# Kernel optimization log

Hardware: AMD Instinct MI355X
Metric: run time of the kernel (lower is better)

## Reference

```python
import jax, jax.numpy as jnp
import numpy as np

N_NODES = 100000
N_EDGES = 3200000
D_NODE = 128
D_EDGE = 16


def setup_inputs() -> dict:
    key = jax.random.key(0)
    k1, k2, k3, k4, k5, k6, k7 = jax.random.split(key, 7)
    nodes = jax.random.normal(k1, (N_NODES, D_NODE), dtype=jnp.float32)
    edges = jax.random.normal(k2, (N_EDGES, D_EDGE), dtype=jnp.float32)
    senders = jax.random.randint(k3, (N_EDGES,), 0, N_NODES, dtype=jnp.int32)
    receivers = jax.random.randint(k4, (N_EDGES,), 0, N_NODES, dtype=jnp.int32)
    w_node = jax.random.normal(k5, (), dtype=jnp.float32)
    w_edge = jax.random.normal(k6, (), dtype=jnp.float32)
    b_node = jax.random.normal(k7, (), dtype=jnp.float32)
    return {
        "nodes": nodes,
        "edges": edges,
        "senders": senders,
        "receivers": receivers,
        "w_node": w_node,
        "w_edge": w_edge,
        "b_node": b_node,
    }


def reference(nodes, edges, senders, receivers, w_node, w_edge, b_node):
    # gather sender node scalar feature (column 0): [E]
    sender_vals = nodes[senders, 0]
    edge_vals = edges[:, 0]  # [E]
    # per-edge message: scalar mult-add
    messages = w_edge * edge_vals + w_node * sender_vals  # [E]
    # scatter-add into receivers: [N]
    agg = jax.ops.segment_sum(messages, receivers, num_segments=nodes.shape[0])
    return w_node * nodes[:, 0] + agg + b_node
```

## Files before the change

kernel.cpp:

```cpp
#include <hip/hip_runtime.h>

#define N_NODES 100000
#define N_EDGES 3200000
#define D_NODE 128
#define D_EDGE 16

__global__ void tmp_init_out(const float* __restrict__ nodes,
                             const float* __restrict__ w_node,
                             const float* __restrict__ b_node,
                             float* __restrict__ out) {
    int i = blockIdx.x * blockDim.x + threadIdx.x;
    if (i < N_NODES) {
        out[i] = w_node[0] * nodes[(size_t)i * D_NODE] + b_node[0];
    }
}

__global__ void tmp_edge_scatter(const float* __restrict__ nodes,
                                 const float* __restrict__ edges,
                                 const int*   __restrict__ senders,
                                 const int*   __restrict__ receivers,
                                 const float* __restrict__ w_node,
                                 const float* __restrict__ w_edge,
                                 float* __restrict__ out) {
    const float wn = w_node[0];
    const float we = w_edge[0];
    int base = (blockIdx.x * blockDim.x + threadIdx.x) * 4;
    if (base + 3 < N_EDGES) {
        int4 s = *(const int4*)(senders + base);
        int4 r = *(const int4*)(receivers + base);
        float e0 = edges[(size_t)(base + 0) * D_EDGE];
        float e1 = edges[(size_t)(base + 1) * D_EDGE];
        float e2 = edges[(size_t)(base + 2) * D_EDGE];
        float e3 = edges[(size_t)(base + 3) * D_EDGE];
        float m0 = we * e0 + wn * nodes[(size_t)s.x * D_NODE];
        float m1 = we * e1 + wn * nodes[(size_t)s.y * D_NODE];
        float m2 = we * e2 + wn * nodes[(size_t)s.z * D_NODE];
        float m3 = we * e3 + wn * nodes[(size_t)s.w * D_NODE];
        atomicAdd(&out[r.x], m0);
        atomicAdd(&out[r.y], m1);
        atomicAdd(&out[r.z], m2);
        atomicAdd(&out[r.w], m3);
    } else {
        for (int e = base; e < N_EDGES; ++e) {
            float m = we * edges[(size_t)e * D_EDGE]
                    + wn * nodes[(size_t)senders[e] * D_NODE];
            atomicAdd(&out[receivers[e]], m);
        }
    }
}

extern "C" void kernel_launch(void* const* d_in, const int* in_sizes, int n_in,
                              void* d_out, int out_size, void* d_ws, size_t ws_size,
                              hipStream_t stream) {
    const float* nodes     = (const float*)d_in[0];
    const float* edges     = (const float*)d_in[1];
    const int*   senders   = (const int*)d_in[2];
    const int*   receivers = (const int*)d_in[3];
    const float* w_node    = (const float*)d_in[4];
    const float* w_edge    = (const float*)d_in[5];
    const float* b_node    = (const float*)d_in[6];
    float* out = (float*)d_out;

    {
        int threads = 256;
        int blocks = (N_NODES + threads - 1) / threads;
        tmp_init_out<<<blocks, threads, 0, stream>>>(nodes, w_node, b_node, out);
    }
    {
        int threads = 256;
        int n_thr = N_EDGES / 4;
        int blocks = (n_thr + threads - 1) / threads;
        tmp_edge_scatter<<<blocks, threads, 0, stream>>>(
            nodes, edges, senders, receivers, w_node, w_edge, out);
    }
}
```

Before: 425.8 us.

## Privatize scatter-add into replicated workspace copies, then reduce

Splits the atomic scatter across up to 16 zero-initialised copies of the output held in workspace, chosen per wavefront, and adds a final kernel that sums the copies with the node term. The aim is to reduce atomic contention on shared receiver addresses. In exchange it adds a zeroing pass and a reduction pass that reads every copy, plus extra memory traffic. It falls back to the original direct path when the workspace is too small.

```diff
diff --git a/kernel.cpp b/kernel.cpp
--- a/kernel.cpp
+++ b/kernel.cpp
@@ -5,26 +5,24 @@
 #define D_NODE 128
 #define D_EDGE 16
 
-__global__ void tmp_init_out(const float* __restrict__ nodes,
-                             const float* __restrict__ w_node,
-                             const float* __restrict__ b_node,
-                             float* __restrict__ out) {
+__global__ void tmp_zero_ws(float4* __restrict__ ws, int n4) {
     int i = blockIdx.x * blockDim.x + threadIdx.x;
-    if (i < N_NODES) {
-        out[i] = w_node[0] * nodes[(size_t)i * D_NODE] + b_node[0];
-    }
+    if (i < n4) ws[i] = make_float4(0.f, 0.f, 0.f, 0.f);
 }
 
-__global__ void tmp_edge_scatter(const float* __restrict__ nodes,
-                                 const float* __restrict__ edges,
-                                 const int*   __restrict__ senders,
-                                 const int*   __restrict__ receivers,
-                                 const float* __restrict__ w_node,
-                                 const float* __restrict__ w_edge,
-                                 float* __restrict__ out) {
+__global__ void tmp_edge_scatter_rep(const float* __restrict__ nodes,
+                                     const float* __restrict__ edges,
+                                     const int*   __restrict__ senders,
+                                     const int*   __restrict__ receivers,
+                                     const float* __restrict__ w_node,
+                                     const float* __restrict__ w_edge,
+                                     float* __restrict__ ws, int rmask) {
     const float wn = w_node[0];
     const float we = w_edge[0];
-    int base = (blockIdx.x * blockDim.x + threadIdx.x) * 4;
+    int t = blockIdx.x * blockDim.x + threadIdx.x;
+    int base = t * 4;
+    if (base >= N_EDGES) return;
+    float* dst = ws + (size_t)((t >> 6) & rmask) * N_NODES;
     if (base + 3 < N_EDGES) {
         int4 s = *(const int4*)(senders + base);
         int4 r = *(const int4*)(receivers + base);
@@ -36,14 +34,63 @@
         float m1 = we * e1 + wn * nodes[(size_t)s.y * D_NODE];
         float m2 = we * e2 + wn * nodes[(size_t)s.z * D_NODE];
         float m3 = we * e3 + wn * nodes[(size_t)s.w * D_NODE];
+        atomicAdd(&dst[r.x], m0);
+        atomicAdd(&dst[r.y], m1);
+        atomicAdd(&dst[r.z], m2);
+        atomicAdd(&dst[r.w], m3);
+    } else {
+        for (int e = base; e < N_EDGES; ++e) {
+            float m = we * edges[(size_t)e * D_EDGE]
+                    + wn * nodes[(size_t)senders[e] * D_NODE];
+            atomicAdd(&dst[receivers[e]], m);
+        }
+    }
+}
+
+__global__ void tmp_reduce_out(const float* __restrict__ nodes,
+                               const float* __restrict__ ws,
+                               const float* __restrict__ w_node,
+                               const float* __restrict__ b_node,
+                               float* __restrict__ out, int nrep) {
+    int i = blockIdx.x * blockDim.x + threadIdx.x;
+    if (i >= N_NODES) return;
+    float s = w_node[0] * nodes[(size_t)i * D_NODE] + b_node[0];
+    for (int r = 0; r < nrep; ++r) s += ws[(size_t)r * N_NODES + i];
+    out[i] = s;
+}
+
+__global__ void tmp_init_out(const float* __restrict__ nodes,
+                             const float* __restrict__ w_node,
+                             const float* __restrict__ b_node,
+                             float* __restrict__ out) {
+    int i = blockIdx.x * blockDim.x + threadIdx.x;
+    if (i < N_NODES) out[i] = w_node[0] * nodes[(size_t)i * D_NODE] + b_node[0];
+}
+
+__global__ void tmp_edge_scatter_direct(const float* __restrict__ nodes,
+                                        const float* __restrict__ edges,
+                                        const int*   __restrict__ senders,
+                                        const int*   __restrict__ receivers,
+                                        const float* __restrict__ w_node,
+                                        const float* __restrict__ w_edge,
+                                        float* __restrict__ out) {
+    const float wn = w_node[0];
+    const float we = w_edge[0];
+    int base = (blockIdx.x * blockDim.x + threadIdx.x) * 4;
+    if (base + 3 < N_EDGES) {
+        int4 s = *(const int4*)(senders + base);
+        int4 r = *(const int4*)(receivers + base);
+        float m0 = we * edges[(size_t)(base + 0) * D_EDGE] + wn * nodes[(size_t)s.x * D_NODE];
+        float m1 = we * edges[(size_t)(base + 1) * D_EDGE] + wn * nodes[(size_t)s.y * D_NODE];
+        float m2 = we * edges[(size_t)(base + 2) * D_EDGE] + wn * nodes[(size_t)s.z * D_NODE];
+        float m3 = we * edges[(size_t)(base + 3) * D_EDGE] + wn * nodes[(size_t)s.w * D_NODE];
         atomicAdd(&out[r.x], m0);
         atomicAdd(&out[r.y], m1);
         atomicAdd(&out[r.z], m2);
         atomicAdd(&out[r.w], m3);
     } else {
         for (int e = base; e < N_EDGES; ++e) {
-            float m = we * edges[(size_t)e * D_EDGE]
-                    + wn * nodes[(size_t)senders[e] * D_NODE];
+            float m = we * edges[(size_t)e * D_EDGE] + wn * nodes[(size_t)senders[e] * D_NODE];
             atomicAdd(&out[receivers[e]], m);
         }
     }
@@ -60,17 +107,41 @@
     const float* w_edge    = (const float*)d_in[5];
     const float* b_node    = (const float*)d_in[6];
     float* out = (float*)d_out;
+    float* ws  = (float*)d_ws;
 
+    int R = 0;
     {
+        size_t per = (size_t)N_NODES * sizeof(float);
+        if (ws_size >= per) {
+            R = 1;
+            while (R < 16 && (size_t)(R * 2) * per <= ws_size) R *= 2;
+        }
+    }
+
+    if (R > 0) {
+        {
+            int n4 = (R * N_NODES) / 4;
+            int threads = 256;
+            tmp_zero_ws<<<(n4 + threads - 1) / threads, threads, 0, stream>>>(
+                (float4*)ws, n4);
+        }
+        {
+            int threads = 256;
+            int n_thr = N_EDGES / 4;
+            tmp_edge_scatter_rep<<<(n_thr + threads - 1) / threads, threads, 0, stream>>>(
+                nodes, edges, senders, receivers, w_node, w_edge, ws, R - 1);
+        }
+        {
+            int threads = 256;
+            tmp_reduce_out<<<(N_NODES + threads - 1) / threads, threads, 0, stream>>>(
+                nodes, ws, w_node, b_node, out, R);
+        }
+    } else {
         int threads = 256;
-        int blocks = (N_NODES + threads - 1) / threads;
-        tmp_init_out<<<blocks, threads, 0, stream>>>(nodes, w_node, b_node, out);
-    }
-    {
-        int threads = 256;
+        tmp_init_out<<<(N_NODES + threads - 1) / threads, threads, 0, stream>>>(
+            nodes, w_node, b_node, out);
         int n_thr = N_EDGES / 4;
-        int blocks = (n_thr + threads - 1) / threads;
-        tmp_edge_scatter<<<blocks, threads, 0, stream>>>(
+        tmp_edge_scatter_direct<<<(n_thr + threads - 1) / threads, threads, 0, stream>>>(
             nodes, edges, senders, receivers, w_node, w_edge, out);
     }
 }
```

After: 427.4 us. Within noise of the previous version (+0.4%).

## Replace global atomic scatter with range-partitioned LDS accumulation and partial reduction

Applied to the files above, without the earlier changes.

Splits the work into four kernels. The first extracts column 0 of the nodes into a compact array. The second computes per-edge messages into a workspace buffer. The third has each block accumulate messages for one 16K-node receiver range in shared memory, using LDS atomics, and write a partial sum. The last sums the partials per node and adds the node term and bias. This removes the random global atomics to the output, at the cost of re-reading receivers and messages once per range and of extra workspace traffic. The new path runs only if the workspace is large enough; otherwise it falls back to the direct atomic kernel.

```diff
diff --git a/kernel.cpp b/kernel.cpp
--- a/kernel.cpp
+++ b/kernel.cpp
@@ -5,46 +5,113 @@
 #define D_NODE 128
 #define D_EDGE 16
 
+#define RANGE_BITS 14
+#define RANGE_SIZE (1 << RANGE_BITS)
+#define RANGE_MASK (RANGE_SIZE - 1)
+#define N_RANGES 7
+
+#define WS_X_OFF    0
+#define WS_MSG_OFF  102400
+#define WS_PART_OFF (102400 + N_EDGES)
+
+__global__ void tmp_k0_extract(const float* __restrict__ nodes,
+                               float* __restrict__ x) {
+    int i = blockIdx.x * blockDim.x + threadIdx.x;
+    if (i < N_NODES) x[i] = nodes[(size_t)i * D_NODE];
+}
+
+__global__ void tmp_k1_messages(const float* __restrict__ x,
+                                const float* __restrict__ edges,
+                                const int*   __restrict__ senders,
+                                const float* __restrict__ w_node,
+                                const float* __restrict__ w_edge,
+                                float* __restrict__ msg) {
+    const float wn = w_node[0];
+    const float we = w_edge[0];
+    int base = (blockIdx.x * blockDim.x + threadIdx.x) * 4;
+    if (base >= N_EDGES) return;
+    int4 s = *(const int4*)(senders + base);
+    float4 m;
+    m.x = we * edges[(size_t)(base + 0) * D_EDGE] + wn * x[s.x];
+    m.y = we * edges[(size_t)(base + 1) * D_EDGE] + wn * x[s.y];
+    m.z = we * edges[(size_t)(base + 2) * D_EDGE] + wn * x[s.z];
+    m.w = we * edges[(size_t)(base + 3) * D_EDGE] + wn * x[s.w];
+    *(float4*)(msg + base) = m;
+}
+
+__global__ void tmp_k2_accum(const float* __restrict__ msg,
+                             const int*   __restrict__ receivers,
+                             float* __restrict__ partials, int nb) {
+    extern __shared__ float acc[];
+    const int range = blockIdx.y;
+    const int slice = blockIdx.x;
+
+    for (int i = threadIdx.x; i < RANGE_SIZE; i += blockDim.x) acc[i] = 0.f;
+    __syncthreads();
+
+    int chunk = (N_EDGES + nb - 1) / nb;
+    chunk = (chunk + 3) & ~3;
+    int start = slice * chunk;
+    int end = start + chunk; if (end > N_EDGES) end = N_EDGES;
+
+    for (int e = start + (int)threadIdx.x * 4; e < end; e += (int)blockDim.x * 4) {
+        int4 r = *(const int4*)(receivers + e);
+        float4 m = *(const float4*)(msg + e);
+        if ((r.x >> RANGE_BITS) == range) atomicAdd(&acc[r.x & RANGE_MASK], m.x);
+        if ((r.y >> RANGE_BITS) == range) atomicAdd(&acc[r.y & RANGE_MASK], m.y);
+        if ((r.z >> RANGE_BITS) == range) atomicAdd(&acc[r.z & RANGE_MASK], m.z);
+        if ((r.w >> RANGE_BITS) == range) atomicAdd(&acc[r.w & RANGE_MASK], m.w);
+    }
+    __syncthreads();
+
+    float* dst = partials + ((size_t)(range * nb + slice) << RANGE_BITS);
+    for (int i = threadIdx.x; i < RANGE_SIZE; i += blockDim.x) dst[i] = acc[i];
+}
+
+__global__ void tmp_k3_reduce(const float* __restrict__ x,
+                              const float* __restrict__ partials,
+                              const float* __restrict__ w_node,
+                              const float* __restrict__ b_node,
+                              float* __restrict__ out, int nb) {
+    int i = blockIdx.x * blockDim.x + threadIdx.x;
+    if (i >= N_NODES) return;
+    int range = i >> RANGE_BITS;
+    int local = i & RANGE_MASK;
+    float s = w_node[0] * x[i] + b_node[0];
+    const float* p = partials + ((size_t)(range * nb) << RANGE_BITS) + local;
+    for (int b = 0; b < nb; ++b) s += p[(size_t)b << RANGE_BITS];
+    out[i] = s;
+}
+
 __global__ void tmp_init_out(const float* __restrict__ nodes,
                              const float* __restrict__ w_node,
                              const float* __restrict__ b_node,
                              float* __restrict__ out) {
     int i = blockIdx.x * blockDim.x + threadIdx.x;
-    if (i < N_NODES) {
-        out[i] = w_node[0] * nodes[(size_t)i * D_NODE] + b_node[0];
-    }
+    if (i < N_NODES) out[i] = w_node[0] * nodes[(size_t)i * D_NODE] + b_node[0];
 }
 
-__global__ void tmp_edge_scatter(const float* __restrict__ nodes,
-                                 const float* __restrict__ edges,
-                                 const int*   __restrict__ senders,
-                                 const int*   __restrict__ receivers,
-                                 const float* __restrict__ w_node,
-                                 const float* __restrict__ w_edge,
-                                 float* __restrict__ out) {
+__global__ void tmp_edge_scatter_direct(const float* __restrict__ nodes,
+                                        const float* __restrict__ edges,
+                                        const int*   __restrict__ senders,
+                                        const int*   __restrict__ receivers,
+                                        const float* __restrict__ w_node,
+                                        const float* __restrict__ w_edge,
+                                        float* __restrict__ out) {
     const float wn = w_node[0];
     const float we = w_edge[0];
     int base = (blockIdx.x * blockDim.x + threadIdx.x) * 4;
     if (base + 3 < N_EDGES) {
         int4 s = *(const int4*)(senders + base);
         int4 r = *(const int4*)(receivers + base);
-        float e0 = edges[(size_t)(base + 0) * D_EDGE];
-        float e1 = edges[(size_t)(base + 1) * D_EDGE];
-        float e2 = edges[(size_t)(base + 2) * D_EDGE];
-        float e3 = edges[(size_t)(base + 3) * D_EDGE];
-        float m0 = we * e0 + wn * nodes[(size_t)s.x * D_NODE];
-        float m1 = we * e1 + wn * nodes[(size_t)s.y * D_NODE];
-        float m2 = we * e2 + wn * nodes[(size_t)s.z * D_NODE];
-        float m3 = we * e3 + wn * nodes[(size_t)s.w * D_NODE];
-        atomicAdd(&out[r.x], m0);
-        atomicAdd(&out[r.y], m1);
-        atomicAdd(&out[r.z], m2);
-        atomicAdd(&out[r.w], m3);
+        atomicAdd(&out[r.x], we * edges[(size_t)(base + 0) * D_EDGE] + wn * nodes[(size_t)s.x * D_NODE]);
+        atomicAdd(&out[r.y], we * edges[(size_t)(base + 1) * D_EDGE] + wn * nodes[(size_t)s.y * D_NODE]);
+        atomicAdd(&out[r.z], we * edges[(size_t)(base + 2) * D_EDGE] + wn * nodes[(size_t)s.z * D_NODE]);
+        atomicAdd(&out[r.w], we * edges[(size_t)(base + 3) * D_EDGE] + wn * nodes[(size_t)s.w * D_NODE]);
     } else {
         for (int e = base; e < N_EDGES; ++e) {
-            float m = we * edges[(size_t)e * D_EDGE]
-                    + wn * nodes[(size_t)senders[e] * D_NODE];
-            atomicAdd(&out[receivers[e]], m);
+            atomicAdd(&out[receivers[e]],
+                      we * edges[(size_t)e * D_EDGE] + wn * nodes[(size_t)senders[e] * D_NODE]);
         }
     }
 }
@@ -60,17 +127,40 @@
     const float* w_edge    = (const float*)d_in[5];
     const float* b_node    = (const float*)d_in[6];
     float* out = (float*)d_out;
+    float* ws  = (float*)d_ws;
 
-    {
+    int nb = 0;
+    for (int cand : {64, 48, 32, 16, 8}) {
+        size_t need = ((size_t)WS_PART_OFF +
+                       (size_t)N_RANGES * cand * RANGE_SIZE) * sizeof(float);
+        if (ws_size >= need) { nb = cand; break; }
+    }
+
+    if (nb > 0) {
+        float* x        = ws + WS_X_OFF;
+        float* msg      = ws + WS_MSG_OFF;
+        float* partials = ws + WS_PART_OFF;
         int threads = 256;
-        int blocks = (N_NODES + threads - 1) / threads;
-        tmp_init_out<<<blocks, threads, 0, stream>>>(nodes, w_node, b_node, out);
-    }
-    {
+
+        tmp_k0_extract<<<(N_NODES + threads - 1) / threads, threads, 0, stream>>>(
+            nodes, x);
+
+        int n_thr = N_EDGES / 4;
+        tmp_k1_messages<<<(n_thr + threads - 1) / threads, threads, 0, stream>>>(
+            x, edges, senders, w_node, w_edge, msg);
+
+        dim3 grid2(nb, N_RANGES);
+        tmp_k2_accum<<<grid2, threads, RANGE_SIZE * sizeof(float), stream>>>(
+            msg, receivers, partials, nb);
+
+        tmp_k3_reduce<<<(N_NODES + threads - 1) / threads, threads, 0, stream>>>(
+            x, partials, w_node, b_node, out, nb);
+    } else {
         int threads = 256;
+        tmp_init_out<<<(N_NODES + threads - 1) / threads, threads, 0, stream>>>(
+            nodes, w_node, b_node, out);
         int n_thr = N_EDGES / 4;
-        int blocks = (n_thr + threads - 1) / threads;
-        tmp_edge_scatter<<<blocks, threads, 0, stream>>>(
+        tmp_edge_scatter_direct<<<(n_thr + threads - 1) / threads, threads, 0, stream>>>(
             nodes, edges, senders, receivers, w_node, w_edge, out);
     }
 }
```

Measured after the change: 388.5 us. -8.7%, faster.
